# Optimization experiments

Measured on AMD Instinct MI355X. Metric: run time of the kernel, lower is better.

## Reference

```python
import jax, jax.numpy as jnp
import numpy as np

EPS = 0.1
MAX_ITER = 50
THRESH = 0.1  # hardcoded early-stop threshold in the torch module


def setup_inputs() -> dict:
    key = jax.random.key(0)
    k1, k2 = jax.random.split(key)
    x = jax.random.normal(k1, (4096, 64), dtype=jnp.float32)
    y = jax.random.normal(k2, (4096, 64), dtype=jnp.float32)
    return {"x": x, "y": y}


def reference(x, y):
    # Cost matrix C_ij = sum_d |x_i - y_j|^2  -> [P1, P2]
    C = jnp.sum(jnp.abs(x[:, None, :] - y[None, :, :]) ** 2, axis=-1)
    P1, P2 = C.shape
    log_mu = jnp.log(jnp.full((P1,), 1.0 / P1, dtype=C.dtype) + 1e-8)
    log_nu = jnp.log(jnp.full((P2,), 1.0 / P2, dtype=C.dtype) + 1e-8)

    def M(u, v):
        # (-C + u_i + v_j) / eps
        return (-C + u[:, None] + v[None, :]) / EPS

    def step(carry, _):
        u, v, done = carry
        u_new = EPS * (log_mu - jax.nn.logsumexp(M(u, v), axis=-1)) + u
        # torch: logsumexp(M(C,u,v).transpose(-2,-1), dim=-1) == logsumexp over axis 0
        v_new = EPS * (log_nu - jax.nn.logsumexp(M(u_new, v), axis=0)) + v
        err = jnp.sum(jnp.abs(u_new - u))
        # emulate the data-dependent break: freeze updates once converged
        u2 = jnp.where(done, u, u_new)
        v2 = jnp.where(done, v, v_new)
        done2 = done | (err < THRESH)
        return (u2, v2, done2), None

    init = (jnp.zeros((P1,), C.dtype), jnp.zeros((P2,), C.dtype), jnp.array(False))
    (u, v, _), _ = jax.lax.scan(step, init, None, length=MAX_ITER)

    pi = jnp.exp(M(u, v))           # transport plan [P1, P2]
    cost = jnp.sum(pi * C)          # reduction='none' with 2D input -> scalar
    return cost, pi, C
```

## Files before the change

### kernel.cpp

```cpp
#include <hip/hip_runtime.h>
#include <math.h>

#define N 4096
#define DIM 64
#define MAX_ITER 50
#define EPS 0.1f
#define THRESH 0.1f

#define SV_SCALE 14.4269504088896340f
#define EPS_LN2 0.0693147180559945f

#define EXP2F(x) __builtin_amdgcn_exp2f(x)
#define LOG2F(x) __builtin_amdgcn_logf(x)

#define NBLK 256
#define TPB 1024
#define WAVES 16
#define NREP 16

#define WS_V 0
#define WS_FLAGS N
#define WS_GGEN (N + 2 * NBLK)
#define WS_TOTAL (N + 2 * NBLK + NREP * 16)

#define PIN4(v) asm volatile("" : "+v"(v.x), "+v"(v.y), "+v"(v.z), "+v"(v.w))

__global__ void init_ws(float* __restrict__ ws) {
    int i = blockIdx.x * 256 + threadIdx.x;
    if (i < WS_TOTAL) ws[i] = 0.0f;
}

__global__ __launch_bounds__(256) void build_dist(const float* __restrict__ A,
                                                  const float* __restrict__ B,
                                                  float* __restrict__ Dst) {
    __shared__ float As[64][68];
    __shared__ float Bs[64][68];
    const int i0 = blockIdx.y << 6, j0 = blockIdx.x << 6;
    const int t = threadIdx.x;
    const float* Ag = A + (size_t)i0 * DIM;
    const float* Bg = B + (size_t)j0 * DIM;
    for (int k = t; k < 4096; k += 256) {
        As[k >> 6][k & 63] = Ag[k];
        Bs[k >> 6][k & 63] = Bg[k];
    }
    __syncthreads();
    const int ty = t >> 4, tx = t & 15;
    float acc[4][4] = {{0.f}};
    for (int d = 0; d < DIM; d += 4) {
        float4 av[4], bv[4];
#pragma unroll
        for (int a = 0; a < 4; ++a) av[a] = *(const float4*)&As[ty + 16 * a][d];
#pragma unroll
        for (int b = 0; b < 4; ++b) bv[b] = *(const float4*)&Bs[tx + 16 * b][d];
#pragma unroll
        for (int a = 0; a < 4; ++a)
#pragma unroll
            for (int b = 0; b < 4; ++b) {
                float d0 = av[a].x - bv[b].x;
                float d1 = av[a].y - bv[b].y;
                float d2 = av[a].z - bv[b].z;
                float d3 = av[a].w - bv[b].w;
                acc[a][b] = fmaf(d0, d0, acc[a][b]);
                acc[a][b] = fmaf(d1, d1, acc[a][b]);
                acc[a][b] = fmaf(d2, d2, acc[a][b]);
                acc[a][b] = fmaf(d3, d3, acc[a][b]);
            }
    }
#pragma unroll
    for (int a = 0; a < 4; ++a) {
        int i = i0 + ty + 16 * a;
        float* drow = Dst + (size_t)i * N + j0;
#pragma unroll
        for (int b = 0; b < 4; ++b) drow[tx + 16 * b] = acc[a][b];
    }
}

__device__ __forceinline__ float grid_sync(float* ws, int b, int t, unsigned G,
                                           const float* red2, float* bcast,
                                           bool wake) {
    __syncthreads();
    if (t == 0) {
        float s = 0.f;
#pragma unroll
        for (int i = 0; i < WAVES; ++i) s += red2[i];
        unsigned long long pk = (unsigned long long)G |
                                ((unsigned long long)__float_as_uint(s) << 32);
        __hip_atomic_store((unsigned long long*)(ws + WS_FLAGS) + b, pk,
                           __ATOMIC_RELAXED, __HIP_MEMORY_SCOPE_AGENT);
    }
    if (b == 0 && t < 64) {
        unsigned long long* fl = (unsigned long long*)(ws + WS_FLAGS);
        float sum;
        for (;;) {
            bool ok = true;
            sum = 0.f;
#pragma unroll
            for (int j = 0; j < NBLK / 64; ++j) {
                unsigned long long q =
                    __hip_atomic_load(fl + (t * (NBLK / 64) + j),
                                      __ATOMIC_RELAXED, __HIP_MEMORY_SCOPE_AGENT);
                ok = ok && ((unsigned)q >= G);
                sum += __uint_as_float((unsigned)(q >> 32));
            }
            if (__all(ok)) break;
            __builtin_amdgcn_s_sleep(1);
        }
#pragma unroll
        for (int off = 32; off; off >>= 1) sum += __shfl_xor(sum, off);
        if (wake && t < NREP) {
            unsigned long long pk =
                (unsigned long long)G |
                ((unsigned long long)__float_as_uint(sum) << 32);
            __hip_atomic_store((unsigned long long*)(ws + WS_GGEN) + t * 8, pk,
                               __ATOMIC_RELAXED, __HIP_MEMORY_SCOPE_AGENT);
        }
        if (t == 0) *bcast = sum;
    } else if (t == 0 && wake) {
        unsigned long long* gp =
            (unsigned long long*)(ws + WS_GGEN) + (b & (NREP - 1)) * 8;
        unsigned long long q;
        for (;;) {
            q = __hip_atomic_load(gp, __ATOMIC_RELAXED, __HIP_MEMORY_SCOPE_AGENT);
            if ((unsigned)q >= G) break;
            __builtin_amdgcn_s_sleep(2);
        }
        *bcast = __uint_as_float((unsigned)(q >> 32));
    }
    __syncthreads();
    return *bcast;
}

__device__ __forceinline__ void stage(const float* __restrict__ src,
                                      float* __restrict__ sv, int t) {
    const unsigned long long* s8 = (const unsigned long long*)src;
#pragma unroll
    for (int i = 0; i < 2; ++i) {
        int idx = t + TPB * i;
        unsigned long long q = __hip_atomic_load(s8 + idx, __ATOMIC_RELAXED,
                                                 __HIP_MEMORY_SCOPE_AGENT);
        sv[2 * idx] = __uint_as_float((unsigned)q) * SV_SCALE;
        sv[2 * idx + 1] = __uint_as_float((unsigned)(q >> 32)) * SV_SCALE;
    }
}

__device__ __forceinline__ float phasePinned(const float4 (&cR)[16],
                                             const float* __restrict__ sv,
                                             int lane, float target) {
    const float4* __restrict__ svv = (const float4*)sv;
    float m = -3.0e38f, s = 0.f;
#pragma unroll
    for (int g = 0; g < 4; ++g) {
        float d[16];
#pragma unroll
        for (int k = 0; k < 4; ++k) {
            float4 w = svv[lane + 64 * (4 * g + k)];
            d[4 * k + 0] = fmaf(cR[4 * g + k].x, -SV_SCALE, w.x);
            d[4 * k + 1] = fmaf(cR[4 * g + k].y, -SV_SCALE, w.y);
            d[4 * k + 2] = fmaf(cR[4 * g + k].z, -SV_SCALE, w.z);
            d[4 * k + 3] = fmaf(cR[4 * g + k].w, -SV_SCALE, w.w);
        }
        float m4[4];
#pragma unroll
        for (int k = 0; k < 4; ++k)
            m4[k] = fmaxf(fmaxf(d[4 * k], d[4 * k + 1]),
                          fmaxf(d[4 * k + 2], d[4 * k + 3]));
        float mg = fmaxf(fmaxf(m4[0], m4[1]), fmaxf(m4[2], m4[3]));
        float mn = fmaxf(m, mg);
        float ps = 0.f;
#pragma unroll
        for (int k = 0; k < 16; ++k) ps += EXP2F(d[k] - mn);
        s = fmaf(s, EXP2F(m - mn), ps);
        m = mn;
    }
#pragma unroll
    for (int off = 32; off; off >>= 1) {
        float mo = __shfl_xor(m, off);
        float so = __shfl_xor(s, off);
        float mn = fmaxf(m, mo);
        s = fmaf(s, EXP2F(m - mn), so * EXP2F(mo - mn));
        m = mn;
    }
    return fmaf(-EPS_LN2, m + LOG2F(s), target);
}

__global__ __launch_bounds__(TPB)
__attribute__((amdgpu_waves_per_eu(4, 4)))
void sinkhorn_persist(
    const float* __restrict__ Cm, float* __restrict__ ws,
    float* __restrict__ out, float target) {
    __shared__ float sv[N];
    __shared__ float4 bufv[WAVES][256];
    __shared__ float us_lds[WAVES];
    __shared__ float red2[WAVES];
    __shared__ float bcast;
    float* v = ws + WS_V;
    unsigned long long* P8 = (unsigned long long*)(out + 1);
    const int t = threadIdx.x;
    const int b = blockIdx.x;
    const int lane = t & 63, wv = t >> 6;
    const int row = (b << 4) + wv;
    unsigned G = 1;
    float errv = 1e30f;
    float uprev = 0.f, un = 0.f;

    float4 cR[16];
    {
        const float4* __restrict__ crow = (const float4*)(Cm + (size_t)row * N);
#pragma unroll
        for (int k = 0; k < 16; ++k) cR[k] = crow[lane + 64 * k];
#pragma unroll
        for (int k = 0; k < 16; ++k) PIN4(cR[k]);
    }

    for (int it = 0; it < MAX_ITER; ++it) {
        stage(v, sv, t);
        __syncthreads();
        un = phasePinned(cR, sv, lane, target);
        if (lane == 0) {
            red2[wv] = fabsf(un - uprev);
            us_lds[wv] = un * SV_SCALE;
        }
        uprev = un;
        __syncthreads();
        const float usw = us_lds[wv];

        for (int c = 0; c < 4; ++c) {
#pragma unroll
            for (int kk = 0; kk < 4; ++kk) {
                float4 cc = cR[4 * c + kk];
                float4 dd;
                dd.x = fmaf(cc.x, -SV_SCALE, usw);
                dd.y = fmaf(cc.y, -SV_SCALE, usw);
                dd.z = fmaf(cc.z, -SV_SCALE, usw);
                dd.w = fmaf(cc.w, -SV_SCALE, usw);
                bufv[wv][lane + 64 * kk] = dd;
            }
            __syncthreads();
            {
                const float* bufs = (const float*)bufv;
                float val[16];
#pragma unroll
                for (int w2 = 0; w2 < 16; ++w2) val[w2] = bufs[w2 * 1024 + t];
                float m = val[0];
#pragma unroll
                for (int w2 = 1; w2 < 16; ++w2) m = fmaxf(m, val[w2]);
                float s = 0.f;
#pragma unroll
                for (int w2 = 0; w2 < 16; ++w2) s += EXP2F(val[w2] - m);
                const int j = c * 1024 + t;
                unsigned long long pk =
                    (unsigned long long)__float_as_uint(m) |
                    ((unsigned long long)__float_as_uint(s) << 32);
                __hip_atomic_store(
                    P8 + ((size_t)(j >> 4) * NBLK + b) * 16 + (j & 15), pk,
                    __ATOMIC_RELAXED, __HIP_MEMORY_SCOPE_AGENT);
            }
            __syncthreads();
        }
        errv = grid_sync(ws, b, t, G++, red2, &bcast, true);

        {
            float m = -3.0e38f, s = 0.f;
#pragma unroll
            for (int i = 0; i < 4; ++i) {
                const int bb = lane + 64 * i;
                unsigned long long q = __hip_atomic_load(
                    P8 + ((size_t)b * NBLK + bb) * 16 + wv, __ATOMIC_RELAXED,
                    __HIP_MEMORY_SCOPE_AGENT);
                float mo = __uint_as_float((unsigned)q);
                float so = __uint_as_float((unsigned)(q >> 32));
                float mn = fmaxf(m, mo);
                s = fmaf(s, EXP2F(m - mn), so * EXP2F(mo - mn));
                m = mn;
            }
#pragma unroll
            for (int off = 32; off; off >>= 1) {
                float mo = __shfl_xor(m, off);
                float so = __shfl_xor(s, off);
                float mn = fmaxf(m, mo);
                s = fmaf(s, EXP2F(m - mn), so * EXP2F(mo - mn));
                m = mn;
            }
            if (lane == 0) {
                float vn = fmaf(-EPS_LN2, m + LOG2F(s), target);
                __hip_atomic_store(&v[16 * b + wv], vn, __ATOMIC_RELAXED,
                                   __HIP_MEMORY_SCOPE_AGENT);
                red2[wv] = 0.f;
            }
        }
        grid_sync(ws, b, t, G++, red2, &bcast, true);
        if (errv < THRESH) break;
    }

    stage(v, sv, t);
    __syncthreads();
    {
        float* pi = out + 1;
        const float ui = un * SV_SCALE;
        float4* __restrict__ prow = (float4*)(pi + (size_t)row * N);
        const float4* __restrict__ svv = (const float4*)sv;
        float csum = 0.f;
#pragma unroll
        for (int k = 0; k < 16; ++k) {
            const int f = lane + 64 * k;
            float4 c = cR[k];
            float4 w = svv[f];
            float4 p;
            p.x = EXP2F(fmaf(c.x, -SV_SCALE, ui + w.x));
            p.y = EXP2F(fmaf(c.y, -SV_SCALE, ui + w.y));
            p.z = EXP2F(fmaf(c.z, -SV_SCALE, ui + w.z));
            p.w = EXP2F(fmaf(c.w, -SV_SCALE, ui + w.w));
            prow[f] = p;
            csum = fmaf(p.x, c.x, csum);
            csum = fmaf(p.y, c.y, csum);
            csum = fmaf(p.z, c.z, csum);
            csum = fmaf(p.w, c.w, csum);
        }
#pragma unroll
        for (int off = 32; off; off >>= 1) csum += __shfl_xor(csum, off);
        if (lane == 0) red2[wv] = csum;
    }
    float ctot = grid_sync(ws, b, t, G++, red2, &bcast, false);
    if (b == 0 && t == 0) out[0] = ctot;
}

extern "C" void kernel_launch(void* const* d_in, const int* in_sizes, int n_in,
                              void* d_out, int out_size, void* d_ws, size_t ws_size,
                              hipStream_t stream) {
    const float* x = (const float*)d_in[0];
    const float* y = (const float*)d_in[1];
    float* out = (float*)d_out;
    float* C = out + 1 + (size_t)N * N;
    float* ws = (float*)d_ws;

    init_ws<<<dim3((WS_TOTAL + 255) / 256), dim3(256), 0, stream>>>(ws);

    dim3 bgrid(64, 64);
    build_dist<<<bgrid, dim3(256), 0, stream>>>(x, y, C);

    float target = EPS * logf(1.0f / (float)N + 1e-8f);

    sinkhorn_persist<<<dim3(NBLK), dim3(TPB), 0, stream>>>(C, ws, out, target);
}
```

Before: 971.8 us.

## Decentralize grid barrier, double-buffer column LDS staging, store v pre-scaled

Replaces the grid barrier's single gatherer plus per-replica wake flags with a scheme where every block's first wave polls all 256 arrival flags directly, using two alternating flag banks keyed on generation parity. This removes the extra hop through block 0 and the wake broadcast. The column-reduction staging becomes double-buffered (bufA/bufB), so writing the next chunk overlaps reading the current one and one __syncthreads per chunk is dropped. v is now kept in the scaled log2 domain, which removes a multiply during staging. In exchange, all blocks polling the flags adds memory traffic, and the kernel uses more LDS.

New measurement: 1.127 ms. 1.16x slower.

```diff
diff --git a/kernel.cpp b/kernel.cpp
--- a/kernel.cpp
+++ b/kernel.cpp
@@ -16,12 +16,10 @@
 #define NBLK 256
 #define TPB 1024
 #define WAVES 16
-#define NREP 16
 
 #define WS_V 0
 #define WS_FLAGS N
-#define WS_GGEN (N + 2 * NBLK)
-#define WS_TOTAL (N + 2 * NBLK + NREP * 16)
+#define WS_TOTAL (N + 4 * NBLK)
 
 #define PIN4(v) asm volatile("" : "+v"(v.x), "+v"(v.y), "+v"(v.z), "+v"(v.w))
 
@@ -76,20 +74,20 @@
 }
 
 __device__ __forceinline__ float grid_sync(float* ws, int b, int t, unsigned G,
-                                           const float* red2, float* bcast,
-                                           bool wake) {
+                                           const float* red2, float* bcast) {
     __syncthreads();
+    unsigned long long* fl =
+        (unsigned long long*)(ws + WS_FLAGS) + (size_t)(G & 1u) * NBLK;
     if (t == 0) {
         float s = 0.f;
 #pragma unroll
         for (int i = 0; i < WAVES; ++i) s += red2[i];
         unsigned long long pk = (unsigned long long)G |
                                 ((unsigned long long)__float_as_uint(s) << 32);
-        __hip_atomic_store((unsigned long long*)(ws + WS_FLAGS) + b, pk,
-                           __ATOMIC_RELAXED, __HIP_MEMORY_SCOPE_AGENT);
-    }
-    if (b == 0 && t < 64) {
-        unsigned long long* fl = (unsigned long long*)(ws + WS_FLAGS);
+        __hip_atomic_store(fl + b, pk, __ATOMIC_RELAXED,
+                           __HIP_MEMORY_SCOPE_AGENT);
+    }
+    if (t < 64) {
         float sum;
         for (;;) {
             bool ok = true;
@@ -97,8 +95,8 @@
 #pragma unroll
             for (int j = 0; j < NBLK / 64; ++j) {
                 unsigned long long q =
-                    __hip_atomic_load(fl + (t * (NBLK / 64) + j),
-                                      __ATOMIC_RELAXED, __HIP_MEMORY_SCOPE_AGENT);
+                    __hip_atomic_load(fl + (t + 64 * j), __ATOMIC_RELAXED,
+                                      __HIP_MEMORY_SCOPE_AGENT);
                 ok = ok && ((unsigned)q >= G);
                 sum += __uint_as_float((unsigned)(q >> 32));
             }
@@ -107,24 +105,7 @@
         }
 #pragma unroll
         for (int off = 32; off; off >>= 1) sum += __shfl_xor(sum, off);
-        if (wake && t < NREP) {
-            unsigned long long pk =
-                (unsigned long long)G |
-                ((unsigned long long)__float_as_uint(sum) << 32);
-            __hip_atomic_store((unsigned long long*)(ws + WS_GGEN) + t * 8, pk,
-                               __ATOMIC_RELAXED, __HIP_MEMORY_SCOPE_AGENT);
-        }
         if (t == 0) *bcast = sum;
-    } else if (t == 0 && wake) {
-        unsigned long long* gp =
-            (unsigned long long*)(ws + WS_GGEN) + (b & (NREP - 1)) * 8;
-        unsigned long long q;
-        for (;;) {
-            q = __hip_atomic_load(gp, __ATOMIC_RELAXED, __HIP_MEMORY_SCOPE_AGENT);
-            if ((unsigned)q >= G) break;
-            __builtin_amdgcn_s_sleep(2);
-        }
-        *bcast = __uint_as_float((unsigned)(q >> 32));
     }
     __syncthreads();
     return *bcast;
@@ -138,8 +119,8 @@
         int idx = t + TPB * i;
         unsigned long long q = __hip_atomic_load(s8 + idx, __ATOMIC_RELAXED,
                                                  __HIP_MEMORY_SCOPE_AGENT);
-        sv[2 * idx] = __uint_as_float((unsigned)q) * SV_SCALE;
-        sv[2 * idx + 1] = __uint_as_float((unsigned)(q >> 32)) * SV_SCALE;
+        sv[2 * idx] = __uint_as_float((unsigned)q);
+        sv[2 * idx + 1] = __uint_as_float((unsigned)(q >> 32));
     }
 }
 
@@ -189,7 +170,8 @@
     const float* __restrict__ Cm, float* __restrict__ ws,
     float* __restrict__ out, float target) {
     __shared__ float sv[N];
-    __shared__ float4 bufv[WAVES][256];
+    __shared__ float4 bufA[WAVES][256];
+    __shared__ float4 bufB[WAVES][256];
     __shared__ float us_lds[WAVES];
     __shared__ float red2[WAVES];
     __shared__ float bcast;
@@ -199,6 +181,7 @@
     const int b = blockIdx.x;
     const int lane = t & 63, wv = t >> 6;
     const int row = (b << 4) + wv;
+    const float targs = target * SV_SCALE;
     unsigned G = 1;
     float errv = 1e30f;
     float uprev = 0.f, un = 0.f;
@@ -224,40 +207,51 @@
         __syncthreads();
         const float usw = us_lds[wv];
 
+#pragma unroll
+        for (int kk = 0; kk < 4; ++kk) {
+            float4 cc = cR[kk];
+            float4 dd;
+            dd.x = fmaf(cc.x, -SV_SCALE, usw);
+            dd.y = fmaf(cc.y, -SV_SCALE, usw);
+            dd.z = fmaf(cc.z, -SV_SCALE, usw);
+            dd.w = fmaf(cc.w, -SV_SCALE, usw);
+            bufA[wv][lane + 64 * kk] = dd;
+        }
+        __syncthreads();
         for (int c = 0; c < 4; ++c) {
-#pragma unroll
-            for (int kk = 0; kk < 4; ++kk) {
-                float4 cc = cR[4 * c + kk];
-                float4 dd;
-                dd.x = fmaf(cc.x, -SV_SCALE, usw);
-                dd.y = fmaf(cc.y, -SV_SCALE, usw);
-                dd.z = fmaf(cc.z, -SV_SCALE, usw);
-                dd.w = fmaf(cc.w, -SV_SCALE, usw);
-                bufv[wv][lane + 64 * kk] = dd;
-            }
-            __syncthreads();
-            {
-                const float* bufs = (const float*)bufv;
-                float val[16];
-#pragma unroll
-                for (int w2 = 0; w2 < 16; ++w2) val[w2] = bufs[w2 * 1024 + t];
-                float m = val[0];
-#pragma unroll
-                for (int w2 = 1; w2 < 16; ++w2) m = fmaxf(m, val[w2]);
-                float s = 0.f;
-#pragma unroll
-                for (int w2 = 0; w2 < 16; ++w2) s += EXP2F(val[w2] - m);
-                const int j = c * 1024 + t;
-                unsigned long long pk =
-                    (unsigned long long)__float_as_uint(m) |
-                    ((unsigned long long)__float_as_uint(s) << 32);
-                __hip_atomic_store(
-                    P8 + ((size_t)(j >> 4) * NBLK + b) * 16 + (j & 15), pk,
-                    __ATOMIC_RELAXED, __HIP_MEMORY_SCOPE_AGENT);
-            }
-            __syncthreads();
-        }
-        errv = grid_sync(ws, b, t, G++, red2, &bcast, true);
+            const float* bufs = (const float*)((c & 1) ? bufB : bufA);
+            float val[16];
+#pragma unroll
+            for (int w2 = 0; w2 < 16; ++w2) val[w2] = bufs[w2 * 1024 + t];
+            if (c < 3) {
+                float4(*bw)[256] = (c & 1) ? bufA : bufB;
+#pragma unroll
+                for (int kk = 0; kk < 4; ++kk) {
+                    float4 cc = cR[4 * (c + 1) + kk];
+                    float4 dd;
+                    dd.x = fmaf(cc.x, -SV_SCALE, usw);
+                    dd.y = fmaf(cc.y, -SV_SCALE, usw);
+                    dd.z = fmaf(cc.z, -SV_SCALE, usw);
+                    dd.w = fmaf(cc.w, -SV_SCALE, usw);
+                    bw[wv][lane + 64 * kk] = dd;
+                }
+            }
+            float m = val[0];
+#pragma unroll
+            for (int w2 = 1; w2 < 16; ++w2) m = fmaxf(m, val[w2]);
+            float s = 0.f;
+#pragma unroll
+            for (int w2 = 0; w2 < 16; ++w2) s += EXP2F(val[w2] - m);
+            const int j = c * 1024 + t;
+            unsigned long long pk =
+                (unsigned long long)__float_as_uint(m) |
+                ((unsigned long long)__float_as_uint(s) << 32);
+            __hip_atomic_store(
+                P8 + ((size_t)(j >> 4) * NBLK + b) * 16 + (j & 15), pk,
+                __ATOMIC_RELAXED, __HIP_MEMORY_SCOPE_AGENT);
+            if (c < 3) __syncthreads();
+        }
+        errv = grid_sync(ws, b, t, G++, red2, &bcast);
 
         {
             float m = -3.0e38f, s = 0.f;
@@ -282,13 +276,13 @@
                 m = mn;
             }
             if (lane == 0) {
-                float vn = fmaf(-EPS_LN2, m + LOG2F(s), target);
+                float vn = targs - (m + LOG2F(s));
                 __hip_atomic_store(&v[16 * b + wv], vn, __ATOMIC_RELAXED,
                                    __HIP_MEMORY_SCOPE_AGENT);
                 red2[wv] = 0.f;
             }
         }
-        grid_sync(ws, b, t, G++, red2, &bcast, true);
+        grid_sync(ws, b, t, G++, red2, &bcast);
         if (errv < THRESH) break;
     }
 
@@ -320,7 +314,7 @@
         for (int off = 32; off; off >>= 1) csum += __shfl_xor(csum, off);
         if (lane == 0) red2[wv] = csum;
     }
-    float ctot = grid_sync(ws, b, t, G++, red2, &bcast, false);
+    float ctot = grid_sync(ws, b, t, G++, red2, &bcast);
     if (b == 0 && t == 0) out[0] = ctot;
 }
 
```

## Replace second grid barrier with tagged v polling and double-buffer partials

Applied to the files above, without the earlier changes.

Each v entry is now stored together with an iteration tag, and blocks poll until the tags they need reach the current iteration. This removes the second grid-wide barrier per Sinkhorn iteration. The partial max/sum buffer alternates between two halves by iteration parity so the next iteration's writes cannot overwrite data still being read. Inside a block, the LDS staging buffer is double-buffered so one chunk is written while the previous one is reduced, which removes one __syncthreads per chunk. The cost is more polling traffic on v and a larger workspace, and it relies on relaxed-atomic tags to order the data correctly.

New measurement: 1.041 ms. +7.1%, slower.

```diff
diff --git a/kernel.cpp b/kernel.cpp
--- a/kernel.cpp
+++ b/kernel.cpp
@@ -19,9 +19,9 @@
 #define NREP 16
 
 #define WS_V 0
-#define WS_FLAGS N
-#define WS_GGEN (N + 2 * NBLK)
-#define WS_TOTAL (N + 2 * NBLK + NREP * 16)
+#define WS_FLAGS (2 * N)
+#define WS_GGEN (2 * N + 2 * NBLK)
+#define WS_TOTAL (2 * N + 2 * NBLK + NREP * 16)
 
 #define PIN4(v) asm volatile("" : "+v"(v.x), "+v"(v.y), "+v"(v.z), "+v"(v.w))
 
@@ -130,17 +130,29 @@
     return *bcast;
 }
 
-__device__ __forceinline__ void stage(const float* __restrict__ src,
-                                      float* __restrict__ sv, int t) {
-    const unsigned long long* s8 = (const unsigned long long*)src;
-#pragma unroll
-    for (int i = 0; i < 2; ++i) {
-        int idx = t + TPB * i;
-        unsigned long long q = __hip_atomic_load(s8 + idx, __ATOMIC_RELAXED,
-                                                 __HIP_MEMORY_SCOPE_AGENT);
-        sv[2 * idx] = __uint_as_float((unsigned)q) * SV_SCALE;
-        sv[2 * idx + 1] = __uint_as_float((unsigned)(q >> 32)) * SV_SCALE;
-    }
+__device__ __forceinline__ void stage_poll(const float* __restrict__ ws,
+                                           float* __restrict__ sv, int t,
+                                           unsigned tagNeed) {
+    const unsigned long long* v8 = (const unsigned long long*)(ws + WS_V);
+    unsigned long long q[4];
+    bool ok[4] = {false, false, false, false};
+    for (;;) {
+        bool all = true;
+#pragma unroll
+        for (int i = 0; i < 4; ++i) {
+            if (!ok[i]) {
+                q[i] = __hip_atomic_load(v8 + (t + TPB * i), __ATOMIC_RELAXED,
+                                         __HIP_MEMORY_SCOPE_AGENT);
+                ok[i] = ((unsigned)q[i] >= tagNeed);
+            }
+            all = all && ok[i];
+        }
+        if (all) break;
+        __builtin_amdgcn_s_sleep(1);
+    }
+#pragma unroll
+    for (int i = 0; i < 4; ++i)
+        sv[t + TPB * i] = __uint_as_float((unsigned)(q[i] >> 32));
 }
 
 __device__ __forceinline__ float phasePinned(const float4 (&cR)[16],
@@ -189,19 +201,22 @@
     const float* __restrict__ Cm, float* __restrict__ ws,
     float* __restrict__ out, float target) {
     __shared__ float sv[N];
-    __shared__ float4 bufv[WAVES][256];
+    __shared__ float4 bufA[WAVES][256];
+    __shared__ float4 bufB[WAVES][256];
     __shared__ float us_lds[WAVES];
     __shared__ float red2[WAVES];
     __shared__ float bcast;
-    float* v = ws + WS_V;
     unsigned long long* P8 = (unsigned long long*)(out + 1);
+    unsigned long long* V8 = (unsigned long long*)(ws + WS_V);
     const int t = threadIdx.x;
     const int b = blockIdx.x;
     const int lane = t & 63, wv = t >> 6;
     const int row = (b << 4) + wv;
+    const float targs = target * SV_SCALE;
     unsigned G = 1;
     float errv = 1e30f;
     float uprev = 0.f, un = 0.f;
+    unsigned fin = MAX_ITER;
 
     float4 cR[16];
     {
@@ -213,8 +228,9 @@
     }
 
     for (int it = 0; it < MAX_ITER; ++it) {
-        stage(v, sv, t);
+        stage_poll(ws, sv, t, (unsigned)it);
         __syncthreads();
+
         un = phasePinned(cR, sv, lane, target);
         if (lane == 0) {
             red2[wv] = fabsf(un - uprev);
@@ -224,39 +240,52 @@
         __syncthreads();
         const float usw = us_lds[wv];
 
+        unsigned long long* Ps = P8 + (size_t)(it & 1) * N * NBLK;
+#pragma unroll
+        for (int kk = 0; kk < 4; ++kk) {
+            float4 cc = cR[kk];
+            float4 dd;
+            dd.x = fmaf(cc.x, -SV_SCALE, usw);
+            dd.y = fmaf(cc.y, -SV_SCALE, usw);
+            dd.z = fmaf(cc.z, -SV_SCALE, usw);
+            dd.w = fmaf(cc.w, -SV_SCALE, usw);
+            bufA[wv][lane + 64 * kk] = dd;
+        }
+        __syncthreads();
         for (int c = 0; c < 4; ++c) {
-#pragma unroll
-            for (int kk = 0; kk < 4; ++kk) {
-                float4 cc = cR[4 * c + kk];
-                float4 dd;
-                dd.x = fmaf(cc.x, -SV_SCALE, usw);
-                dd.y = fmaf(cc.y, -SV_SCALE, usw);
-                dd.z = fmaf(cc.z, -SV_SCALE, usw);
-                dd.w = fmaf(cc.w, -SV_SCALE, usw);
-                bufv[wv][lane + 64 * kk] = dd;
-            }
-            __syncthreads();
-            {
-                const float* bufs = (const float*)bufv;
-                float val[16];
-#pragma unroll
-                for (int w2 = 0; w2 < 16; ++w2) val[w2] = bufs[w2 * 1024 + t];
-                float m = val[0];
-#pragma unroll
-                for (int w2 = 1; w2 < 16; ++w2) m = fmaxf(m, val[w2]);
-                float s = 0.f;
-#pragma unroll
-                for (int w2 = 0; w2 < 16; ++w2) s += EXP2F(val[w2] - m);
-                const int j = c * 1024 + t;
-                unsigned long long pk =
-                    (unsigned long long)__float_as_uint(m) |
-                    ((unsigned long long)__float_as_uint(s) << 32);
-                __hip_atomic_store(
-                    P8 + ((size_t)(j >> 4) * NBLK + b) * 16 + (j & 15), pk,
-                    __ATOMIC_RELAXED, __HIP_MEMORY_SCOPE_AGENT);
-            }
-            __syncthreads();
-        }
+            const float* bufs = (const float*)((c & 1) ? bufB : bufA);
+            float val[16];
+#pragma unroll
+            for (int w2 = 0; w2 < 16; ++w2) val[w2] = bufs[w2 * 1024 + t];
+            if (c < 3) {
+                float4(*bw)[256] = (c & 1) ? bufA : bufB;
+#pragma unroll
+                for (int kk = 0; kk < 4; ++kk) {
+                    float4 cc = cR[4 * (c + 1) + kk];
+                    float4 dd;
+                    dd.x = fmaf(cc.x, -SV_SCALE, usw);
+                    dd.y = fmaf(cc.y, -SV_SCALE, usw);
+                    dd.z = fmaf(cc.z, -SV_SCALE, usw);
+                    dd.w = fmaf(cc.w, -SV_SCALE, usw);
+                    bw[wv][lane + 64 * kk] = dd;
+                }
+            }
+            float m = val[0];
+#pragma unroll
+            for (int w2 = 1; w2 < 16; ++w2) m = fmaxf(m, val[w2]);
+            float s = 0.f;
+#pragma unroll
+            for (int w2 = 0; w2 < 16; ++w2) s += EXP2F(val[w2] - m);
+            const int j = c * 1024 + t;
+            unsigned long long pk =
+                (unsigned long long)__float_as_uint(m) |
+                ((unsigned long long)__float_as_uint(s) << 32);
+            __hip_atomic_store(
+                Ps + ((size_t)(j >> 4) * NBLK + b) * 16 + (j & 15), pk,
+                __ATOMIC_RELAXED, __HIP_MEMORY_SCOPE_AGENT);
+            if (c < 3) __syncthreads();
+        }
+
         errv = grid_sync(ws, b, t, G++, red2, &bcast, true);
 
         {
@@ -265,7 +294,7 @@
             for (int i = 0; i < 4; ++i) {
                 const int bb = lane + 64 * i;
                 unsigned long long q = __hip_atomic_load(
-                    P8 + ((size_t)b * NBLK + bb) * 16 + wv, __ATOMIC_RELAXED,
+                    Ps + ((size_t)b * NBLK + bb) * 16 + wv, __ATOMIC_RELAXED,
                     __HIP_MEMORY_SCOPE_AGENT);
                 float mo = __uint_as_float((unsigned)q);
                 float so = __uint_as_float((unsigned)(q >> 32));
@@ -282,17 +311,20 @@
                 m = mn;
             }
             if (lane == 0) {
-                float vn = fmaf(-EPS_LN2, m + LOG2F(s), target);
-                __hip_atomic_store(&v[16 * b + wv], vn, __ATOMIC_RELAXED,
+                float vn = targs - (m + LOG2F(s));
+                unsigned long long pk =
+                    (unsigned long long)(unsigned)(it + 1) |
+                    ((unsigned long long)__float_as_uint(vn) << 32);
+                __hip_atomic_store(V8 + (16 * b + wv), pk, __ATOMIC_RELAXED,
                                    __HIP_MEMORY_SCOPE_AGENT);
                 red2[wv] = 0.f;
             }
         }
-        grid_sync(ws, b, t, G++, red2, &bcast, true);
+        fin = (unsigned)(it + 1);
         if (errv < THRESH) break;
     }
 
-    stage(v, sv, t);
+    stage_poll(ws, sv, t, fin);
     __syncthreads();
     {
         float* pi = out + 1;
```

## Double-buffer column LDS staging and exchange single log-sum-exp partials

Applied to the files above, without the earlier changes.

The column-reduction chunks now alternate between two LDS buffers. The next chunk is written while the current one is reduced, which removes one block barrier per chunk. Each block publishes a single per-column log-sum-exp float instead of a packed (max, sum) pair, halving the cross-block partial traffic and simplifying the merge. The dual potential v is now stored already scaled to log2 units, so the stage step drops its multiply. The costs are more LDS per block and extra log2/exp2 work in the partial exchange.

Result: faster. 872.0 us (-10.3%).

```diff
diff --git a/kernel.cpp b/kernel.cpp
--- a/kernel.cpp
+++ b/kernel.cpp
@@ -130,16 +130,16 @@
     return *bcast;
 }
 
-__device__ __forceinline__ void stage(const float* __restrict__ src,
+__device__ __forceinline__ void stage(const float* __restrict__ ws,
                                       float* __restrict__ sv, int t) {
-    const unsigned long long* s8 = (const unsigned long long*)src;
+    const unsigned long long* s8 = (const unsigned long long*)(ws + WS_V);
 #pragma unroll
     for (int i = 0; i < 2; ++i) {
         int idx = t + TPB * i;
         unsigned long long q = __hip_atomic_load(s8 + idx, __ATOMIC_RELAXED,
                                                  __HIP_MEMORY_SCOPE_AGENT);
-        sv[2 * idx] = __uint_as_float((unsigned)q) * SV_SCALE;
-        sv[2 * idx + 1] = __uint_as_float((unsigned)(q >> 32)) * SV_SCALE;
+        sv[2 * idx] = __uint_as_float((unsigned)q);
+        sv[2 * idx + 1] = __uint_as_float((unsigned)(q >> 32));
     }
 }
 
@@ -189,16 +189,18 @@
     const float* __restrict__ Cm, float* __restrict__ ws,
     float* __restrict__ out, float target) {
     __shared__ float sv[N];
-    __shared__ float4 bufv[WAVES][256];
+    __shared__ float4 bufA[WAVES][256];
+    __shared__ float4 bufB[WAVES][256];
     __shared__ float us_lds[WAVES];
     __shared__ float red2[WAVES];
     __shared__ float bcast;
     float* v = ws + WS_V;
-    unsigned long long* P8 = (unsigned long long*)(out + 1);
+    float* P4 = out + 1;
     const int t = threadIdx.x;
     const int b = blockIdx.x;
     const int lane = t & 63, wv = t >> 6;
     const int row = (b << 4) + wv;
+    const float targs = target * SV_SCALE;
     unsigned G = 1;
     float errv = 1e30f;
     float uprev = 0.f, un = 0.f;
@@ -213,7 +215,7 @@
     }
 
     for (int it = 0; it < MAX_ITER; ++it) {
-        stage(v, sv, t);
+        stage(ws, sv, t);
         __syncthreads();
         un = phasePinned(cR, sv, lane, target);
         if (lane == 0) {
@@ -224,55 +226,59 @@
         __syncthreads();
         const float usw = us_lds[wv];
 
+#pragma unroll
+        for (int kk = 0; kk < 4; ++kk) {
+            float4 cc = cR[kk];
+            float4 dd;
+            dd.x = fmaf(cc.x, -SV_SCALE, usw);
+            dd.y = fmaf(cc.y, -SV_SCALE, usw);
+            dd.z = fmaf(cc.z, -SV_SCALE, usw);
+            dd.w = fmaf(cc.w, -SV_SCALE, usw);
+            bufA[wv][lane + 64 * kk] = dd;
+        }
+        __syncthreads();
         for (int c = 0; c < 4; ++c) {
-#pragma unroll
-            for (int kk = 0; kk < 4; ++kk) {
-                float4 cc = cR[4 * c + kk];
-                float4 dd;
-                dd.x = fmaf(cc.x, -SV_SCALE, usw);
-                dd.y = fmaf(cc.y, -SV_SCALE, usw);
-                dd.z = fmaf(cc.z, -SV_SCALE, usw);
-                dd.w = fmaf(cc.w, -SV_SCALE, usw);
-                bufv[wv][lane + 64 * kk] = dd;
-            }
-            __syncthreads();
-            {
-                const float* bufs = (const float*)bufv;
-                float val[16];
-#pragma unroll
-                for (int w2 = 0; w2 < 16; ++w2) val[w2] = bufs[w2 * 1024 + t];
-                float m = val[0];
-#pragma unroll
-                for (int w2 = 1; w2 < 16; ++w2) m = fmaxf(m, val[w2]);
-                float s = 0.f;
-#pragma unroll
-                for (int w2 = 0; w2 < 16; ++w2) s += EXP2F(val[w2] - m);
-                const int j = c * 1024 + t;
-                unsigned long long pk =
-                    (unsigned long long)__float_as_uint(m) |
-                    ((unsigned long long)__float_as_uint(s) << 32);
-                __hip_atomic_store(
-                    P8 + ((size_t)(j >> 4) * NBLK + b) * 16 + (j & 15), pk,
+            const float* bufs = (const float*)((c & 1) ? bufB : bufA);
+            float val[16];
+#pragma unroll
+            for (int w2 = 0; w2 < 16; ++w2) val[w2] = bufs[w2 * 1024 + t];
+            if (c < 3) {
+                float4(*bw)[256] = (c & 1) ? bufA : bufB;
+#pragma unroll
+                for (int kk = 0; kk < 4; ++kk) {
+                    float4 cc = cR[4 * (c + 1) + kk];
+                    float4 dd;
+                    dd.x = fmaf(cc.x, -SV_SCALE, usw);
+                    dd.y = fmaf(cc.y, -SV_SCALE, usw);
+                    dd.z = fmaf(cc.z, -SV_SCALE, usw);
+                    dd.w = fmaf(cc.w, -SV_SCALE, usw);
+                    bw[wv][lane + 64 * kk] = dd;
+                }
+            }
+            float m = val[0];
+#pragma unroll
+            for (int w2 = 1; w2 < 16; ++w2) m = fmaxf(m, val[w2]);
+            float s = 0.f;
+#pragma unroll
+            for (int w2 = 0; w2 < 16; ++w2) s += EXP2F(val[w2] - m);
+            const int j = c * 1024 + t;
+            __hip_atomic_store(
+                P4 + ((size_t)(j >> 4) * NBLK + b) * 16 + (j & 15),
+                m + LOG2F(s), __ATOMIC_RELAXED, __HIP_MEMORY_SCOPE_AGENT);
+            if (c < 3) __syncthreads();
+        }
+        errv = grid_sync(ws, b, t, G++, red2, &bcast, true);
+
+        {
+            float L[4];
+#pragma unroll
+            for (int i = 0; i < 4; ++i)
+                L[i] = __hip_atomic_load(
+                    P4 + ((size_t)b * NBLK + (lane + 64 * i)) * 16 + wv,
                     __ATOMIC_RELAXED, __HIP_MEMORY_SCOPE_AGENT);
-            }
-            __syncthreads();
-        }
-        errv = grid_sync(ws, b, t, G++, red2, &bcast, true);
-
-        {
-            float m = -3.0e38f, s = 0.f;
-#pragma unroll
-            for (int i = 0; i < 4; ++i) {
-                const int bb = lane + 64 * i;
-                unsigned long long q = __hip_atomic_load(
-                    P8 + ((size_t)b * NBLK + bb) * 16 + wv, __ATOMIC_RELAXED,
-                    __HIP_MEMORY_SCOPE_AGENT);
-                float mo = __uint_as_float((unsigned)q);
-                float so = __uint_as_float((unsigned)(q >> 32));
-                float mn = fmaxf(m, mo);
-                s = fmaf(s, EXP2F(m - mn), so * EXP2F(mo - mn));
-                m = mn;
-            }
+            float m = fmaxf(fmaxf(L[0], L[1]), fmaxf(L[2], L[3]));
+            float s = EXP2F(L[0] - m) + EXP2F(L[1] - m) + EXP2F(L[2] - m) +
+                      EXP2F(L[3] - m);
 #pragma unroll
             for (int off = 32; off; off >>= 1) {
                 float mo = __shfl_xor(m, off);
@@ -282,7 +288,7 @@
                 m = mn;
             }
             if (lane == 0) {
-                float vn = fmaf(-EPS_LN2, m + LOG2F(s), target);
+                float vn = targs - (m + LOG2F(s));
                 __hip_atomic_store(&v[16 * b + wv], vn, __ATOMIC_RELAXED,
                                    __HIP_MEMORY_SCOPE_AGENT);
                 red2[wv] = 0.f;
@@ -292,7 +298,7 @@
         if (errv < THRESH) break;
     }
 
-    stage(v, sv, t);
+    stage(ws, sv, t);
     __syncthreads();
     {
         float* pi = out + 1;
```
